# Performance work log

Hardware: AMD Instinct MI355X
Metric: run time of the kernel (lower is better)

## Reference

```python
import jax, jax.numpy as jnp
import numpy as np
import math

MUL = 64
N_EDGES = 100000
# (multiplicity, l, parity)
IRREPS_IN1 = [(MUL, 0, 1), (MUL, 1, -1), (MUL, 2, 1)]
IRREPS_IN2 = [(1, 0, 1), (1, 1, -1), (1, 2, 1)]
IRREPS_OUT = [(MUL, 0, 1), (MUL, 1, -1), (MUL, 2, 1)]


def _su2_cg(j1, j2, j3, m1, m2, m3):
    # Racah formula (integer l only here)
    if m3 != m1 + m2:
        return 0.0
    vmin = max(-j1 + j2 + m3, -j1 + m1, 0)
    vmax = min(j2 + j3 + m1, j3 - j1 + j2, j3 + m3)
    f = math.factorial
    c = math.sqrt((2 * j3 + 1) * f(j3 + j1 - j2) * f(j3 - j1 + j2) * f(j1 + j2 - j3)
                  * f(j3 + m3) * f(j3 - m3)
                  / (f(j1 + j2 + j3 + 1) * f(j1 - m1) * f(j1 + m1) * f(j2 - m2) * f(j2 + m2)))
    s = 0.0
    for v in range(vmin, vmax + 1):
        s += (-1) ** (v + j2 + m2) * f(j2 + j3 + m1 - v) * f(j1 - m1 + v) / (
            f(v) * f(j3 - j1 + j2 - v) * f(j3 + m3 - v) * f(j1 - j2 - m3 + v))
    return c * s


def _su2_cg_tensor(j1, j2, j3):
    C = np.zeros((2 * j1 + 1, 2 * j2 + 1, 2 * j3 + 1))
    for m1 in range(-j1, j1 + 1):
        for m2 in range(-j2, j2 + 1):
            m3 = m1 + m2
            if abs(m3) <= j3:
                C[j1 + m1, j2 + m2, j3 + m3] = _su2_cg(j1, j2, j3, m1, m2, m3)
    return C


def _change_basis(l):
    # complex -> real spherical-harmonic change of basis (e3nn convention)
    q = np.zeros((2 * l + 1, 2 * l + 1), dtype=np.complex128)
    for m in range(-l, 0):
        q[l + m, l + abs(m)] = 1 / math.sqrt(2)
        q[l + m, l - abs(m)] = -1j / math.sqrt(2)
    q[l, l] = 1.0
    for m in range(1, l + 1):
        q[l + m, l + abs(m)] = (-1) ** m / math.sqrt(2)
        q[l + m, l - abs(m)] = 1j * (-1) ** m / math.sqrt(2)
    return ((-1j) ** l) * q


def _real_w3j(l1, l2, l3):
    C = np.einsum('ai,bj,ck,abc->ijk', _change_basis(l1), _change_basis(l2),
                  np.conj(_change_basis(l3)),
                  _su2_cg_tensor(l1, l2, l3).astype(np.complex128))
    C = np.real(C)
    n = np.linalg.norm(C)
    return C / n if n > 0 else C  # unit Frobenius norm, as e3nn wigner_3j


def _build():
    # replicates get_feasible_tp for mode 'uvw'
    mid = []   # (mul_out, l, p)
    raw = []   # (i, j, k, l1, l2, l3)
    for i, (mu1, l1, p1) in enumerate(IRREPS_IN1):
        for j, (mu2, l2, p2) in enumerate(IRREPS_IN2):
            for l3 in range(abs(l1 - l2), l1 + l2 + 1):
                p3 = p1 * p2
                mul_out = sum(m for (m, ll, pp) in IRREPS_OUT if ll == l3 and pp == p3)
                if mul_out == 0:
                    continue
                key = (mul_out, l3, p3)
                if key not in mid:
                    mid.append(key)
                raw.append((i, j, mid.index(key), l1, l2, l3))
    # (mid is already sorted 0e,1o,2e for these irreps)
    instrs = []
    off = 0
    for (i, j, k, l1, l2, l3) in raw:
        fan = sum(IRREPS_IN1[a][0] * IRREPS_IN2[b][0] for (a, b, kk, _, _, _) in raw if kk == k)
        alpha = math.sqrt((2 * l3 + 1) / fan)  # path normalization from get_feasible_tp
        u, v, w = IRREPS_IN1[i][0], IRREPS_IN2[j][0], mid[k][0]
        instrs.append(dict(i=i, j=j, k=k, alpha=alpha, C=_real_w3j(l1, l2, l3),
                           u=u, v=v, w=w, off=off))
        off += u * v * w
    return mid, instrs, off


IRREPS_MID, INSTRS, WEIGHT_NUMEL = _build()
IN1_OFF = np.cumsum([0] + [m * (2 * l + 1) for m, l, _ in IRREPS_IN1]).tolist()
IN2_OFF = np.cumsum([0] + [m * (2 * l + 1) for m, l, _ in IRREPS_IN2]).tolist()
DIM_IN1 = IN1_OFF[-1]
DIM_IN2 = IN2_OFF[-1]


def _tp(x, y, weights):
    # fully-connected ('uvw') segmented CG tensor product; post_linear is Identity
    N = x.shape[0]
    outs = [jnp.zeros((N, m * (2 * l + 1)), x.dtype) for (m, l, _) in IRREPS_MID]
    for ins in INSTRS:
        i, j, k = ins['i'], ins['j'], ins['k']
        mu1, l1, _ = IRREPS_IN1[i]
        mu2, l2, _ = IRREPS_IN2[j]
        xi = x[:, IN1_OFF[i]:IN1_OFF[i + 1]].reshape(N, mu1, 2 * l1 + 1)
        yj = y[:, IN2_OFF[j]:IN2_OFF[j + 1]].reshape(N, mu2, 2 * l2 + 1)
        W = weights[ins['off']:ins['off'] + ins['u'] * ins['v'] * ins['w']]
        W = W.reshape(ins['u'], ins['v'], ins['w'])
        C = jnp.asarray(ins['C'], x.dtype)  # [2l1+1, 2l2+1, 2l3+1]
        r = ins['alpha'] * jnp.einsum('uvw,pqr,nup,nvq->nwr', W, C, xi, yj)
        outs[k] = outs[k] + r.reshape(N, -1)
    return jnp.concatenate(outs, axis=1)


def setup_inputs() -> dict:
    key = jax.random.key(0)
    k1, k2, k3 = jax.random.split(key, 3)
    x = jax.random.normal(k1, (N_EDGES, DIM_IN1), jnp.float32)
    y = jax.random.normal(k2, (N_EDGES, DIM_IN2), jnp.float32)
    weights = jax.random.normal(k3, (WEIGHT_NUMEL,), jnp.float32) / math.sqrt(WEIGHT_NUMEL)
    return {'x': x, 'y': y, 'weights': weights}


def reference(x, y, weights):
    return _tp(x, y, weights)
```

## Files before the change

### kernel.cpp

```cpp
#include <hip/hip_runtime.h>
#include <hip/hip_bf16.h>
#include <stdint.h>


#define NEDGES 100000
#define NE_W   16
#define NBLK   (NEDGES/NE_W)

typedef short    short8 __attribute__((ext_vector_type(8)));
typedef float    f32x4  __attribute__((ext_vector_type(4)));
typedef uint32_t u32x4  __attribute__((ext_vector_type(4)));

constexpr int L1A[11] = {0,0,0,1,1,1,1,2,2,2,2};
constexpr int L2A[11] = {0,1,2,0,1,1,2,0,1,2,2};
constexpr int L3A[11] = {0,1,2,1,0,2,1,2,1,0,2};

constexpr double cfact(int n){ double r=1.0; for(int i=2;i<=n;++i) r*=(double)i; return r; }
constexpr double csqrt(double x){ if(x<=0.0) return 0.0; double g = x>1.0?x:1.0;
                                 for(int i=0;i<80;++i) g=0.5*(g+x/g); return g; }
constexpr int imax2(int a,int b){return a>b?a:b;}
constexpr int imin2(int a,int b){return a<b?a:b;}

constexpr double su2_cg(int j1,int j2,int j3,int m1,int m2,int m3){
  if(m3 != m1+m2) return 0.0;
  int vmin = imax2(imax2(-j1+j2+m3, -j1+m1), 0);
  int vmax = imin2(imin2(j2+j3+m1, j3-j1+j2), j3+m3);
  double c = csqrt((double)(2*j3+1)*cfact(j3+j1-j2)*cfact(j3-j1+j2)*cfact(j1+j2-j3)
                   *cfact(j3+m3)*cfact(j3-m3)
                   /(cfact(j1+j2+j3+1)*cfact(j1-m1)*cfact(j1+m1)*cfact(j2-m2)*cfact(j2+m2)));
  double s=0.0;
  for(int v=vmin; v<=vmax; ++v){
    double sg = ((v+j2+m2)&1)? -1.0 : 1.0;
    s += sg*cfact(j2+j3+m1-v)*cfact(j1-m1+v)
         /(cfact(v)*cfact(j3-j1+j2-v)*cfact(j3+m3-v)*cfact(j1-j2-m3+v));
  }
  return c*s;
}

struct Cplx{ double re, im; };
struct Q55 { Cplx q[5][5]; };

constexpr Q55 change_basis(int l){
  Q55 Q{};
  const double is2 = 1.0/csqrt(2.0);
  for(int m=-l;m<0;++m){
    Q.q[l+m][l-m].re =  is2;
    Q.q[l+m][l+m].im = -is2;
  }
  Q.q[l][l].re = 1.0;
  for(int m=1;m<=l;++m){
    double s = (m&1)? -1.0 : 1.0;
    Q.q[l+m][l+m].re = s*is2;
    Q.q[l+m][l-m].im = s*is2;
  }
  for(int i=0;i<5;++i) for(int j=0;j<5;++j){
    double re=Q.q[i][j].re, im=Q.q[i][j].im;
    if(l==1){ Q.q[i][j].re = im;  Q.q[i][j].im = -re; }
    else if(l==2){ Q.q[i][j].re = -re; Q.q[i][j].im = -im; }
  }
  return Q;
}

struct Tbl {
  double C[11][5][5][5];
  double alpha[11];
};

constexpr Tbl build_tbl(){
  Tbl T{};
  for(int I=0;I<11;++I){
    const int l1=L1A[I], l2=L2A[I], l3=L3A[I];
    const int D1=2*l1+1, D2=2*l2+1, D3=2*l3+1;
    double cg[5][5][5]{};
    for(int a=0;a<D1;++a)for(int b=0;b<D2;++b){
      int m3 = (a-l1)+(b-l2);
      if(m3>=-l3 && m3<=l3) cg[a][b][l3+m3] = su2_cg(l1,l2,l3,a-l1,b-l2,m3);
    }
    Q55 q1 = change_basis(l1), q2 = change_basis(l2), q3 = change_basis(l3);
    Cplx T1[5][5][5]{};
    for(int i=0;i<D1;++i)for(int b=0;b<D2;++b)for(int c=0;c<D3;++c){
      double re=0,im=0;
      for(int a=0;a<D1;++a){ re += q1.q[a][i].re*cg[a][b][c]; im += q1.q[a][i].im*cg[a][b][c]; }
      T1[i][b][c].re=re; T1[i][b][c].im=im;
    }
    Cplx T2[5][5][5]{};
    for(int i=0;i<D1;++i)for(int j=0;j<D2;++j)for(int c=0;c<D3;++c){
      double re=0,im=0;
      for(int b=0;b<D2;++b){
        double qr=q2.q[b][j].re, qi=q2.q[b][j].im;
        re += qr*T1[i][b][c].re - qi*T1[i][b][c].im;
        im += qr*T1[i][b][c].im + qi*T1[i][b][c].re;
      }
      T2[i][j][c].re=re; T2[i][j][c].im=im;
    }
    double nrm2 = 0.0;
    for(int i=0;i<D1;++i)for(int j=0;j<D2;++j)for(int k=0;k<D3;++k){
      double re=0;
      for(int c=0;c<D3;++c){
        double qr=q3.q[c][k].re, qi=-q3.q[c][k].im;
        re += qr*T2[i][j][c].re - qi*T2[i][j][c].im;
      }
      T.C[I][i][j][k] = re; nrm2 += re*re;
    }
    double nrm = csqrt(nrm2);
    if(nrm > 0.0)
      for(int i=0;i<D1;++i)for(int j=0;j<D2;++j)for(int k=0;k<D3;++k) T.C[I][i][j][k] /= nrm;
    const int fan = (l3==0)?192:256;
    T.alpha[I] = csqrt((double)(2*l3+1)/(double)fan);
  }
  return T;
}

constexpr Tbl TBL = build_tbl();

__device__ const float c_alpha[11] = {
  (float)TBL.alpha[0],(float)TBL.alpha[1],(float)TBL.alpha[2],(float)TBL.alpha[3],
  (float)TBL.alpha[4],(float)TBL.alpha[5],(float)TBL.alpha[6],(float)TBL.alpha[7],
  (float)TBL.alpha[8],(float)TBL.alpha[9],(float)TBL.alpha[10]
};

__device__ __forceinline__ uint16_t f2bf(float f){
  uint32_t u = __float_as_uint(f);
  return (uint16_t)((u + 0x7fffu + ((u>>16)&1u)) >> 16);
}
__device__ __forceinline__ uint32_t pk2c(float a, float b){
  __hip_bfloat162 h = __float22bfloat162_rn(float2{a,b});
  uint32_t r; __builtin_memcpy(&r, &h, 4); return r;
}

__global__ __launch_bounds__(256) void prep_w(const float* __restrict__ w,
                                              uint16_t* __restrict__ wt){
  int tid = blockIdx.x*256 + threadIdx.x;
  if(tid >= 11*4096) return;
  int I = tid >> 12;
  int rem = tid & 4095;
  int wo = rem >> 6, u = rem & 63;
  wt[tid] = f2bf(c_alpha[I] * w[(I<<12) + (u<<6) + wo]);
}


template<int I>
__device__ __forceinline__ void load_B(short8 B[2][4], const uint16_t* __restrict__ wt,
                                       int lmod, int ldiv){
  #pragma unroll
  for(int ks=0;ks<2;++ks)
    #pragma unroll
    for(int nt=0;nt<4;++nt)
      B[ks][nt] = *(const short8*)(wt + (I*64 + nt*16 + lmod)*64 + ks*32 + ldiv*8);
}

template<int I>
__device__ __forceinline__ void do_instr_pre(f32x4* acc, const short8 B[2][4],
                                             const char* xsw, const float* yv,
                                             int lmod, int ldiv)
{
  constexpr int l1=L1A[I], l2=L2A[I], l3=L3A[I];
  constexpr int D1=2*l1+1, D2=2*l2+1, D3=2*l3+1;
  constexpr int PB=(l1==0)?0:((l1==1)?1:4);
  constexpr int QB=(l2==0)?0:((l2==1)?1:4);

  float M[D1][D3];
  #pragma unroll
  for(int p=0;p<D1;++p)
    #pragma unroll
    for(int r=0;r<D3;++r){
      float m=0.f;
      #pragma unroll
      for(int q=0;q<D2;++q){
        const float cc = (float)TBL.C[I][p][q][r];
        if(cc != 0.0f) m = fmaf(cc, yv[QB+q], m);
      }
      M[p][r]=m;
    }

  #pragma unroll
  for(int ks=0;ks<2;++ks){
    float xf[D1][8];
    #pragma unroll
    for(int p=0;p<D1;++p){
      const int rho  = lmod*9 + PB + p;
      const int addr = rho*128 + (((ks*4+ldiv) ^ (rho&7))<<4);
      const u32x4 xv = *(const u32x4*)(xsw + addr);
      #pragma unroll
      for(int k=0;k<4;++k){
        xf[p][2*k]   = __uint_as_float(xv[k]<<16);
        xf[p][2*k+1] = __uint_as_float(xv[k]&0xffff0000u);
      }
    }
    #pragma unroll
    for(int rt=0;rt<D3;++rt){
      float zf[8];
      #pragma unroll
      for(int i=0;i<8;++i) zf[i]=0.f;
      #pragma unroll
      for(int p=0;p<D1;++p)
        #pragma unroll
        for(int i=0;i<8;++i) zf[i] = fmaf(M[p][rt], xf[p][i], zf[i]);
      u32x4 av = { pk2c(zf[0],zf[1]), pk2c(zf[2],zf[3]),
                   pk2c(zf[4],zf[5]), pk2c(zf[6],zf[7]) };
      const short8 A = *(const short8*)&av;
      #pragma unroll
      for(int nt=0;nt<4;++nt)
        acc[rt*4+nt] = __builtin_amdgcn_mfma_f32_16x16x32_bf16(A, B[ks][nt], acc[rt*4+nt], 0,0,0);
    }
  }
}

template<int I>
__device__ __forceinline__ void chain1(f32x4* acc, const short8 B[2][4],
                                       const uint16_t* __restrict__ wt,
                                       const char* xsw, const float* yv,
                                       int lmod, int ldiv){
  do_instr_pre<I>(acc, B, xsw, yv, lmod, ldiv);
}

template<int I, int J, int... Rest>
__device__ __forceinline__ void chain1(f32x4* acc, const short8 B[2][4],
                                       const uint16_t* __restrict__ wt,
                                       const char* xsw, const float* yv,
                                       int lmod, int ldiv){
  short8 Bn[2][4];
  load_B<J>(Bn, wt, lmod, ldiv);
  __builtin_amdgcn_sched_barrier(0);
  do_instr_pre<I>(acc, B, xsw, yv, lmod, ldiv);
  chain1<J, Rest...>(acc, Bn, wt, xsw, yv, lmod, ldiv);
}

template<int KOFF, int D3, int IF, int... Is>
__device__ __forceinline__ void kgroup(const uint16_t* __restrict__ wt, const char* xsw,
                                       const float* yv, float* __restrict__ outb,
                                       float* __restrict__ ost, int lane,
                                       int lmod, int ldiv)
{
  constexpr int LEN    = 64*D3;
  constexpr int STRIDE = LEN + 4;
  f32x4 acc[D3*4];
  #pragma unroll
  for(int i=0;i<D3*4;++i) acc[i] = (f32x4){0.f,0.f,0.f,0.f};

  short8 B0[2][4];
  load_B<IF>(B0, wt, lmod, ldiv);
  __builtin_amdgcn_sched_barrier(0);
  chain1<IF, Is...>(acc, B0, wt, xsw, yv, lmod, ldiv);

  #pragma unroll
  for(int rt=0; rt<D3; ++rt)
    #pragma unroll
    for(int nt=0;nt<4;++nt)
      #pragma unroll
      for(int j=0;j<4;++j)
        ost[(ldiv*4+j)*STRIDE + (nt*16+lmod)*D3 + rt] = acc[rt*4+nt][j];
  __syncthreads();

  const int es2 = lane>>2, oct2 = lane&3;
  #pragma unroll
  for(int c=0;c<LEN/16;++c){
    *(float4*)(outb + (long)es2*576 + KOFF + c*16 + oct2*4) =
      *(const float4*)(ost + es2*STRIDE + c*16 + oct2*4);
  }
  __syncthreads();
}

template<int KOFF, int D3, int IF, int... Is>
__device__ __forceinline__ void kgroup_split(const uint16_t* __restrict__ wt, const char* xsw,
                                             const float* yv, float* __restrict__ outb,
                                             float* __restrict__ ost, int lane,
                                             int lmod, int ldiv)
{
  constexpr int LENH   = 32*D3;
  constexpr int STRIDE = LENH + 4;
  f32x4 acc[D3*4];
  #pragma unroll
  for(int i=0;i<D3*4;++i) acc[i] = (f32x4){0.f,0.f,0.f,0.f};

  short8 B0[2][4];
  load_B<IF>(B0, wt, lmod, ldiv);
  __builtin_amdgcn_sched_barrier(0);
  chain1<IF, Is...>(acc, B0, wt, xsw, yv, lmod, ldiv);

  const int es2 = lane>>2, oct2 = lane&3;
  #pragma unroll
  for(int h=0; h<2; ++h){
    #pragma unroll
    for(int rt=0; rt<D3; ++rt)
      #pragma unroll
      for(int ntl=0; ntl<2; ++ntl)
        #pragma unroll
        for(int j=0;j<4;++j)
          ost[(ldiv*4+j)*STRIDE + (ntl*16+lmod)*D3 + rt] = acc[rt*4 + h*2+ntl][j];
    __syncthreads();

    #pragma unroll
    for(int c=0;c<LENH/16;++c){
      *(float4*)(outb + (long)es2*576 + KOFF + h*LENH + c*16 + oct2*4) =
        *(const float4*)(ost + es2*STRIDE + c*16 + oct2*4);
    }
    __syncthreads();
  }
}

__global__ __launch_bounds__(64,2) void tp_main(const float* __restrict__ x,
                                                const float* __restrict__ y,
                                                const uint16_t* __restrict__ wt,
                                                float* __restrict__ out)
{
  __shared__ char  xlds[18432] __attribute__((aligned(16)));
  __shared__ float ost[3136]   __attribute__((aligned(16)));
  const int lane = threadIdx.x & 63;
  const int lmod = lane&15, ldiv = lane>>4;
  const long nE = (long)blockIdx.x*NE_W;
  char* xsw = xlds;

  float yv[9];
  {
    const float* yp = y + (nE + lmod)*9;
    #pragma unroll
    for(int q=0;q<9;++q) yv[q] = yp[q];
  }

  {
    const int es = lane>>2, q4 = lane&3;
    const float* xr = x + (nE+es)*576;

    {
      float f0[16];
      #pragma unroll
      for(int i=0;i<4;++i){ float4 v = *(const float4*)(xr + q4*16 + 4*i);
        f0[4*i]=v.x; f0[4*i+1]=v.y; f0[4*i+2]=v.z; f0[4*i+3]=v.w; }
      uint32_t xp[8];
      #pragma unroll
      for(int a=0;a<8;++a) xp[a] = pk2c(f0[2*a], f0[2*a+1]);
      const int rho = es*9;
      char* base = xsw + rho*128;
      *(u32x4*)(base + (((2*q4  ) ^ (rho&7))<<4)) = *(const u32x4*)&xp[0];
      *(u32x4*)(base + (((2*q4+1) ^ (rho&7))<<4)) = *(const u32x4*)&xp[4];
    }
    {
      float f1[48];
      #pragma unroll
      for(int i=0;i<12;++i){ float4 v = *(const float4*)(xr + 64 + q4*48 + 4*i);
        f1[4*i]=v.x; f1[4*i+1]=v.y; f1[4*i+2]=v.z; f1[4*i+3]=v.w; }
      #pragma unroll
      for(int p=0;p<3;++p){
        uint32_t xp[8];
        #pragma unroll
        for(int a=0;a<8;++a) xp[a] = pk2c(f1[(2*a)*3+p], f1[(2*a+1)*3+p]);
        const int rho = es*9 + 1 + p;
        char* base = xsw + rho*128;
        *(u32x4*)(base + (((2*q4  ) ^ (rho&7))<<4)) = *(const u32x4*)&xp[0];
        *(u32x4*)(base + (((2*q4+1) ^ (rho&7))<<4)) = *(const u32x4*)&xp[4];
      }
    }
    {
      float f2[80];
      #pragma unroll
      for(int i=0;i<20;++i){ float4 v = *(const float4*)(xr + 256 + q4*80 + 4*i);
        f2[4*i]=v.x; f2[4*i+1]=v.y; f2[4*i+2]=v.z; f2[4*i+3]=v.w; }
      #pragma unroll
      for(int p=0;p<5;++p){
        uint32_t xp[8];
        #pragma unroll
        for(int a=0;a<8;++a) xp[a] = pk2c(f2[(2*a)*5+p], f2[(2*a+1)*5+p]);
        const int rho = es*9 + 4 + p;
        char* base = xsw + rho*128;
        *(u32x4*)(base + (((2*q4  ) ^ (rho&7))<<4)) = *(const u32x4*)&xp[0];
        *(u32x4*)(base + (((2*q4+1) ^ (rho&7))<<4)) = *(const u32x4*)&xp[4];
      }
    }
  }

  __syncthreads();

  float* outb = out + nE*576;
  kgroup<0,   1, 0,4,9   >(wt, xsw, yv, outb, ost, lane, lmod, ldiv);
  kgroup<64,  3, 1,3,6,8 >(wt, xsw, yv, outb, ost, lane, lmod, ldiv);
  kgroup_split<256, 5, 2,5,7,10>(wt, xsw, yv, outb, ost, lane, lmod, ldiv);
}

extern "C" void kernel_launch(void* const* d_in, const int* in_sizes, int n_in,
                              void* d_out, int out_size, void* d_ws, size_t ws_size,
                              hipStream_t stream)
{
  const float* x = (const float*)d_in[0];
  const float* y = (const float*)d_in[1];
  const float* w = (const float*)d_in[2];
  uint16_t* wt = (uint16_t*)d_ws;
  prep_w<<<176, 256, 0, stream>>>(w, wt);
  tp_main<<<NBLK, 64, 0, stream>>>(x, y, wt, (float*)d_out);
}
```

Baseline: 142.4 us.

## Split output groups across two waves per block with per-wave staging

The block grows from one wave to two. Wave 0 computes the l=0 and l=1 output groups, and wave 1 computes the l=2 group in quarter chunks. The x load and bf16 swizzle into LDS now use all 128 threads. Each wave has its own LDS staging buffer, so the block-wide barriers in the output path become per-wave waitcnt fences. This aims to raise parallelism and cut serial latency per block, but the work is unevenly split between the waves (roughly 7 MFMA instruction chains versus 4) and the l=2 group now needs more staging rounds.

Measured after the change: 130.3 us. -8.5%, faster.

```diff
diff --git a/kernel.cpp b/kernel.cpp
--- a/kernel.cpp
+++ b/kernel.cpp
@@ -127,6 +127,10 @@
   __hip_bfloat162 h = __float22bfloat162_rn(float2{a,b});
   uint32_t r; __builtin_memcpy(&r, &h, 4); return r;
 }
+__device__ __forceinline__ void wave_fence(){
+  asm volatile("s_waitcnt vmcnt(0) lgkmcnt(0)" ::: "memory");
+  __builtin_amdgcn_sched_barrier(0);
+}
 
 __global__ __launch_bounds__(256) void prep_w(const float* __restrict__ w,
                                               uint16_t* __restrict__ wt){
@@ -226,22 +230,28 @@
   chain1<J, Rest...>(acc, Bn, wt, xsw, yv, lmod, ldiv);
 }
 
-template<int KOFF, int D3, int IF, int... Is>
-__device__ __forceinline__ void kgroup(const uint16_t* __restrict__ wt, const char* xsw,
-                                       const float* yv, float* __restrict__ outb,
-                                       float* __restrict__ ost, int lane,
-                                       int lmod, int ldiv)
-{
-  constexpr int LEN    = 64*D3;
-  constexpr int STRIDE = LEN + 4;
-  f32x4 acc[D3*4];
+template<int D3, int IF, int... Is>
+__device__ __forceinline__ void run_chain(f32x4* acc, const uint16_t* __restrict__ wt,
+                                          const char* xsw, const float* yv,
+                                          int lmod, int ldiv){
   #pragma unroll
   for(int i=0;i<D3*4;++i) acc[i] = (f32x4){0.f,0.f,0.f,0.f};
-
   short8 B0[2][4];
   load_B<IF>(B0, wt, lmod, ldiv);
   __builtin_amdgcn_sched_barrier(0);
   chain1<IF, Is...>(acc, B0, wt, xsw, yv, lmod, ldiv);
+}
+
+template<int KOFF, int D3, int IF, int... Is>
+__device__ __forceinline__ void kgroup_full(const uint16_t* __restrict__ wt, const char* xsw,
+                                            const float* yv, float* __restrict__ outb,
+                                            float* __restrict__ ost, int lane,
+                                            int lmod, int ldiv)
+{
+  constexpr int LEN    = 64*D3;
+  constexpr int STRIDE = LEN + 4;
+  f32x4 acc[D3*4];
+  run_chain<D3, IF, Is...>(acc, wt, xsw, yv, lmod, ldiv);
 
   #pragma unroll
   for(int rt=0; rt<D3; ++rt)
@@ -250,7 +260,7 @@
       #pragma unroll
       for(int j=0;j<4;++j)
         ost[(ldiv*4+j)*STRIDE + (nt*16+lmod)*D3 + rt] = acc[rt*4+nt][j];
-  __syncthreads();
+  wave_fence();
 
   const int es2 = lane>>2, oct2 = lane&3;
   #pragma unroll
@@ -258,25 +268,19 @@
     *(float4*)(outb + (long)es2*576 + KOFF + c*16 + oct2*4) =
       *(const float4*)(ost + es2*STRIDE + c*16 + oct2*4);
   }
-  __syncthreads();
+  wave_fence();
 }
 
 template<int KOFF, int D3, int IF, int... Is>
-__device__ __forceinline__ void kgroup_split(const uint16_t* __restrict__ wt, const char* xsw,
-                                             const float* yv, float* __restrict__ outb,
-                                             float* __restrict__ ost, int lane,
-                                             int lmod, int ldiv)
+__device__ __forceinline__ void kgroup_h(const uint16_t* __restrict__ wt, const char* xsw,
+                                         const float* yv, float* __restrict__ outb,
+                                         float* __restrict__ ost, int lane,
+                                         int lmod, int ldiv)
 {
   constexpr int LENH   = 32*D3;
   constexpr int STRIDE = LENH + 4;
   f32x4 acc[D3*4];
-  #pragma unroll
-  for(int i=0;i<D3*4;++i) acc[i] = (f32x4){0.f,0.f,0.f,0.f};
-
-  short8 B0[2][4];
-  load_B<IF>(B0, wt, lmod, ldiv);
-  __builtin_amdgcn_sched_barrier(0);
-  chain1<IF, Is...>(acc, B0, wt, xsw, yv, lmod, ldiv);
+  run_chain<D3, IF, Is...>(acc, wt, xsw, yv, lmod, ldiv);
 
   const int es2 = lane>>2, oct2 = lane&3;
   #pragma unroll
@@ -288,25 +292,55 @@
         #pragma unroll
         for(int j=0;j<4;++j)
           ost[(ldiv*4+j)*STRIDE + (ntl*16+lmod)*D3 + rt] = acc[rt*4 + h*2+ntl][j];
-    __syncthreads();
-
+    wave_fence();
     #pragma unroll
     for(int c=0;c<LENH/16;++c){
       *(float4*)(outb + (long)es2*576 + KOFF + h*LENH + c*16 + oct2*4) =
         *(const float4*)(ost + es2*STRIDE + c*16 + oct2*4);
     }
-    __syncthreads();
-  }
-}
-
-__global__ __launch_bounds__(64,2) void tp_main(const float* __restrict__ x,
-                                                const float* __restrict__ y,
-                                                const uint16_t* __restrict__ wt,
-                                                float* __restrict__ out)
+    wave_fence();
+  }
+}
+
+template<int KOFF, int D3, int IF, int... Is>
+__device__ __forceinline__ void kgroup_q(const uint16_t* __restrict__ wt, const char* xsw,
+                                         const float* yv, float* __restrict__ outb,
+                                         float* __restrict__ ost, int lane,
+                                         int lmod, int ldiv)
+{
+  constexpr int LENQ   = 16*D3;
+  constexpr int STRIDE = LENQ + 4;
+  f32x4 acc[D3*4];
+  run_chain<D3, IF, Is...>(acc, wt, xsw, yv, lmod, ldiv);
+
+  const int es2 = lane>>2, oct2 = lane&3;
+  #pragma unroll
+  for(int q=0; q<4; ++q){
+    #pragma unroll
+    for(int rt=0; rt<D3; ++rt)
+      #pragma unroll
+      for(int j=0;j<4;++j)
+        ost[(ldiv*4+j)*STRIDE + lmod*D3 + rt] = acc[rt*4 + q][j];
+    wave_fence();
+    #pragma unroll
+    for(int c=0;c<LENQ/16;++c){
+      *(float4*)(outb + (long)es2*576 + KOFF + q*LENQ + c*16 + oct2*4) =
+        *(const float4*)(ost + es2*STRIDE + c*16 + oct2*4);
+    }
+    wave_fence();
+  }
+}
+
+__global__ __launch_bounds__(128,2) void tp_main(const float* __restrict__ x,
+                                                 const float* __restrict__ y,
+                                                 const uint16_t* __restrict__ wt,
+                                                 float* __restrict__ out)
 {
   __shared__ char  xlds[18432] __attribute__((aligned(16)));
-  __shared__ float ost[3136]   __attribute__((aligned(16)));
-  const int lane = threadIdx.x & 63;
+  __shared__ float ost0[1600]  __attribute__((aligned(16)));
+  __shared__ float ost1[1344]  __attribute__((aligned(16)));
+  const int tid  = threadIdx.x;
+  const int wave = tid>>6, lane = tid&63;
   const int lmod = lane&15, ldiv = lane>>4;
   const long nE = (long)blockIdx.x*NE_W;
   char* xsw = xlds;
@@ -319,62 +353,51 @@
   }
 
   {
-    const int es = lane>>2, q4 = lane&3;
+    const int es = tid>>3, oct = tid&7;
     const float* xr = x + (nE+es)*576;
-
+    uint32_t xp[9][4];
+
+    const float4 a0 = *(const float4*)(xr + oct*8);
+    const float4 a1 = *(const float4*)(xr + oct*8 + 4);
+    xp[0][0]=pk2c(a0.x,a0.y); xp[0][1]=pk2c(a0.z,a0.w);
+    xp[0][2]=pk2c(a1.x,a1.y); xp[0][3]=pk2c(a1.z,a1.w);
+    float f1[24];
     {
-      float f0[16];
-      #pragma unroll
-      for(int i=0;i<4;++i){ float4 v = *(const float4*)(xr + q4*16 + 4*i);
-        f0[4*i]=v.x; f0[4*i+1]=v.y; f0[4*i+2]=v.z; f0[4*i+3]=v.w; }
-      uint32_t xp[8];
-      #pragma unroll
-      for(int a=0;a<8;++a) xp[a] = pk2c(f0[2*a], f0[2*a+1]);
-      const int rho = es*9;
-      char* base = xsw + rho*128;
-      *(u32x4*)(base + (((2*q4  ) ^ (rho&7))<<4)) = *(const u32x4*)&xp[0];
-      *(u32x4*)(base + (((2*q4+1) ^ (rho&7))<<4)) = *(const u32x4*)&xp[4];
-    }
+      const float4* p1 = (const float4*)(xr + 64 + oct*24);
+      #pragma unroll
+      for(int i=0;i<6;++i){ float4 v=p1[i]; f1[4*i]=v.x; f1[4*i+1]=v.y; f1[4*i+2]=v.z; f1[4*i+3]=v.w; }
+    }
+    #pragma unroll
+    for(int p=0;p<3;++p)
+      #pragma unroll
+      for(int a=0;a<4;++a) xp[1+p][a] = pk2c(f1[(2*a)*3+p], f1[(2*a+1)*3+p]);
+    float f2[40];
     {
-      float f1[48];
-      #pragma unroll
-      for(int i=0;i<12;++i){ float4 v = *(const float4*)(xr + 64 + q4*48 + 4*i);
-        f1[4*i]=v.x; f1[4*i+1]=v.y; f1[4*i+2]=v.z; f1[4*i+3]=v.w; }
-      #pragma unroll
-      for(int p=0;p<3;++p){
-        uint32_t xp[8];
-        #pragma unroll
-        for(int a=0;a<8;++a) xp[a] = pk2c(f1[(2*a)*3+p], f1[(2*a+1)*3+p]);
-        const int rho = es*9 + 1 + p;
-        char* base = xsw + rho*128;
-        *(u32x4*)(base + (((2*q4  ) ^ (rho&7))<<4)) = *(const u32x4*)&xp[0];
-        *(u32x4*)(base + (((2*q4+1) ^ (rho&7))<<4)) = *(const u32x4*)&xp[4];
-      }
-    }
-    {
-      float f2[80];
-      #pragma unroll
-      for(int i=0;i<20;++i){ float4 v = *(const float4*)(xr + 256 + q4*80 + 4*i);
-        f2[4*i]=v.x; f2[4*i+1]=v.y; f2[4*i+2]=v.z; f2[4*i+3]=v.w; }
-      #pragma unroll
-      for(int p=0;p<5;++p){
-        uint32_t xp[8];
-        #pragma unroll
-        for(int a=0;a<8;++a) xp[a] = pk2c(f2[(2*a)*5+p], f2[(2*a+1)*5+p]);
-        const int rho = es*9 + 4 + p;
-        char* base = xsw + rho*128;
-        *(u32x4*)(base + (((2*q4  ) ^ (rho&7))<<4)) = *(const u32x4*)&xp[0];
-        *(u32x4*)(base + (((2*q4+1) ^ (rho&7))<<4)) = *(const u32x4*)&xp[4];
-      }
+      const float4* p2 = (const float4*)(xr + 256 + oct*40);
+      #pragma unroll
+      for(int i=0;i<10;++i){ float4 v=p2[i]; f2[4*i]=v.x; f2[4*i+1]=v.y; f2[4*i+2]=v.z; f2[4*i+3]=v.w; }
+    }
+    #pragma unroll
+    for(int p=0;p<5;++p)
+      #pragma unroll
+      for(int a=0;a<4;++a) xp[4+p][a] = pk2c(f2[(2*a)*5+p], f2[(2*a+1)*5+p]);
+
+    #pragma unroll
+    for(int pidx=0;pidx<9;++pidx){
+      const int rho = es*9 + pidx;
+      *(u32x4*)(xsw + rho*128 + ((oct ^ (rho&7))<<4)) = *(const u32x4*)&xp[pidx][0];
     }
   }
 
   __syncthreads();
 
   float* outb = out + nE*576;
-  kgroup<0,   1, 0,4,9   >(wt, xsw, yv, outb, ost, lane, lmod, ldiv);
-  kgroup<64,  3, 1,3,6,8 >(wt, xsw, yv, outb, ost, lane, lmod, ldiv);
-  kgroup_split<256, 5, 2,5,7,10>(wt, xsw, yv, outb, ost, lane, lmod, ldiv);
+  if(wave == 0){
+    kgroup_full<0,  1, 0,4,9   >(wt, xsw, yv, outb, ost0, lane, lmod, ldiv);
+    kgroup_h   <64, 3, 1,3,6,8 >(wt, xsw, yv, outb, ost0, lane, lmod, ldiv);
+  } else {
+    kgroup_q   <256,5, 2,5,7,10>(wt, xsw, yv, outb, ost1, lane, lmod, ldiv);
+  }
 }
 
 extern "C" void kernel_launch(void* const* d_in, const int* in_sizes, int n_in,
@@ -386,5 +409,5 @@
   const float* w = (const float*)d_in[2];
   uint16_t* wt = (uint16_t*)d_ws;
   prep_w<<<176, 256, 0, stream>>>(w, wt);
-  tp_main<<<NBLK, 64, 0, stream>>>(x, y, wt, (float*)d_out);
-}
+  tp_main<<<NBLK, 128, 0, stream>>>(x, y, wt, (float*)d_out);
+}
```
